# Kernel tuning notes

Hardware: AMD Instinct MI355X
Metric: run time of the kernel (lower is better)

The kernel has to match this reference:

```python
import jax, jax.numpy as jnp
import numpy as np

B, C, N, K = 2, 64, 16384, 16
C_OUT = 64


def setup_inputs() -> dict:
    key = jax.random.key(0)
    k1, k2, k3, k4 = jax.random.split(key, 4)
    x = jax.random.normal(k1, (B, C, N), dtype=jnp.float32)
    edge_index = jax.random.randint(k2, (2, B, N, K), 0, N, dtype=jnp.int64)
    # 1x1 Conv2d params: weight [C_out, 3C], bias [C_out]
    W = jax.random.normal(k3, (C_OUT, 3 * C), dtype=jnp.float32) * (1.0 / np.sqrt(3 * C))
    b = jax.random.normal(k4, (C_OUT,), dtype=jnp.float32) * 0.01
    return {"x": x, "edge_index": edge_index, "W": W, "b": b}


def _gather_nodes(x, idx):
    # x: [B, C, N], idx: [B, N, K] -> [B, C, N, K]
    return jax.vmap(lambda xb, ib: xb[:, ib])(x, idx)


def reference(x, edge_index, W, b):
    # x: [B, C, N]; edge_index: [2, B, N, K]
    x_i = _gather_nodes(x, edge_index[1])          # center features  [B,C,N,K]
    x_j = _gather_nodes(x, edge_index[0])          # neighbor features [B,C,N,K]
    edge_features = x_j - x_i                      # [B,C,N,K]
    global_feature = jnp.mean(x, axis=2, keepdims=True)  # [B,C,1] global mean over nodes
    global_rep = jnp.broadcast_to(global_feature[..., None], x_i.shape)  # [B,C,N,K]
    combined = jnp.concatenate([x_i, edge_features, global_rep], axis=1)  # [B,3C,N,K]
    # BasicConv: 1x1 conv + ReLU (norm=None)
    out = jnp.einsum("bcnk,oc->bonk", combined, W) + b[None, :, None, None]
    out = jax.nn.relu(out)
    return jnp.max(out, axis=-1, keepdims=True)    # [B,C_out,N,1]
```

## Files before the change

### kernel.cpp

```cpp
#include <hip/hip_runtime.h>
#include <hip/hip_bf16.h>


#define NNODES 16384
#define NCH 64

typedef _Float16 half4 __attribute__((ext_vector_type(4)));

__global__ __launch_bounds__(256) void mean_kernel(const float* __restrict__ x,
                                                   float* __restrict__ g) {
  int row = blockIdx.x;
  const float4* x4 = (const float4*)(x + (size_t)row * NNODES);
  int t = threadIdx.x;
  float s = 0.f;
#pragma unroll
  for (int i = 0; i < 16; ++i) {
    float4 q = x4[t + i * 256];
    s += (q.x + q.y) + (q.z + q.w);
  }
#pragma unroll
  for (int off = 32; off > 0; off >>= 1) s += __shfl_down(s, off, 64);
  __shared__ float wsum[4];
  int lane = t & 63, wv = t >> 6;
  if (lane == 0) wsum[wv] = s;
  __syncthreads();
  if (t == 0) g[row] = (wsum[0] + wsum[1] + wsum[2] + wsum[3]) * (1.0f / 16384.0f);
}

__global__ __launch_bounds__(128) void gmat_kernel(const float* __restrict__ W,
                                                   const float* __restrict__ bias,
                                                   const float* __restrict__ g,
                                                   float* __restrict__ G) {
  int t = threadIdx.x;
  int b = t >> 6, o = t & 63;
  float s = bias[o];
  const float* w3 = W + o * 192 + 128;
  const float* gb = g + b * 64;
#pragma unroll
  for (int c = 0; c < 64; ++c) s += w3[c] * gb[c];
  G[t] = s;
}

__global__ __launch_bounds__(256) void uv_kernel(const float* __restrict__ x,
                                                 const float* __restrict__ W,
                                                 _Float16* __restrict__ u,
                                                 _Float16* __restrict__ v) {
  __shared__ float A[64][64];
  __shared__ float Bm[64][64];
  int t = threadIdx.x;
  {
    int o = t & 63, c0 = (t >> 6) * 16;
    const float* wr = W + o * 192;
#pragma unroll
    for (int i = 0; i < 16; ++i) {
      int c = c0 + i;
      float w1 = wr[c], w2 = wr[64 + c];
      A[c][o] = w1 - w2;
      Bm[c][o] = w2;
    }
  }
  __syncthreads();
  int lane = t & 63;
  int wv = __builtin_amdgcn_readfirstlane(t >> 6);
  int blk = blockIdx.x;
  int b = blk >> 9;
  int m0 = (blk & 511) * 32 + wv * 8;
  const float* xb = x + (size_t)b * (NCH * NNODES) + m0;
  float aU[8], aV[8];
#pragma unroll
  for (int i = 0; i < 8; ++i) { aU[i] = 0.f; aV[i] = 0.f; }
#pragma unroll 8
  for (int c = 0; c < 64; ++c) {
    float a = A[c][lane];
    float bb = Bm[c][lane];
    const float4* xr = (const float4*)(xb + (size_t)c * NNODES);
    float4 q0 = xr[0];
    float4 q1 = xr[1];
    aU[0] += a * q0.x; aV[0] += bb * q0.x;
    aU[1] += a * q0.y; aV[1] += bb * q0.y;
    aU[2] += a * q0.z; aV[2] += bb * q0.z;
    aU[3] += a * q0.w; aV[3] += bb * q0.w;
    aU[4] += a * q1.x; aV[4] += bb * q1.x;
    aU[5] += a * q1.y; aV[5] += bb * q1.y;
    aU[6] += a * q1.z; aV[6] += bb * q1.z;
    aU[7] += a * q1.w; aV[7] += bb * q1.w;
  }
  _Float16* ub = u + ((size_t)b * NNODES + m0) * NCH + lane;
  _Float16* vb = v + ((size_t)b * NNODES + m0) * NCH + lane;
#pragma unroll
  for (int i = 0; i < 8; ++i) {
    ub[i * NCH] = (_Float16)aU[i];
    vb[i * NCH] = (_Float16)aV[i];
  }
}

__global__ __launch_bounds__(256) void gather_kernel(const int* __restrict__ ei,
                                                     const _Float16* __restrict__ u,
                                                     const _Float16* __restrict__ v,
                                                     const float* __restrict__ G,
                                                     float* __restrict__ out) {
  __shared__ float tile[64][17];
  int t = threadIdx.x;
  int lane = t & 63;
  int wv = t >> 6;
  int blk = blockIdx.x;
  int xcd = blk & 7;
  int b = xcd >> 2;
  int nb = (blk >> 3) * 4 + (xcd & 3);
  int n0 = nb * 16;
  int node_q = lane >> 4;
  int k_l = lane & 15;
  int n = n0 + wv * 4 + node_q;
  const int* e0b = ei + (size_t)b * NNODES * 16;
  const int* e1b = ei + (size_t)(2 + b) * NNODES * 16;
  int idx0 = e0b[n * 16 + k_l];
  int idx1 = e1b[n * 16 + k_l];
  int c4 = k_l * 4;
  const half4* ub = (const half4*)(u + (size_t)b * NNODES * NCH + c4);
  const half4* vb = (const half4*)(v + (size_t)b * NNODES * NCH + c4);
  half4 acc;
  acc.x = acc.y = acc.z = acc.w = (_Float16)(-60000.0f);
#pragma unroll
  for (int k = 0; k < 16; ++k) {
    int src = (lane & 48) + k;
    int m1 = __shfl(idx1, src, 64);
    int m0 = __shfl(idx0, src, 64);
    half4 a = ub[(size_t)m1 * 16];
    half4 bb = vb[(size_t)m0 * 16];
    half4 s = a + bb;
    acc = __builtin_elementwise_max(acc, s);
  }
  float4 Gl = *(const float4*)(G + b * 64 + c4);
  int nn = wv * 4 + node_q;
  tile[c4 + 0][nn] = fmaxf((float)acc.x + Gl.x, 0.0f);
  tile[c4 + 1][nn] = fmaxf((float)acc.y + Gl.y, 0.0f);
  tile[c4 + 2][nn] = fmaxf((float)acc.z + Gl.z, 0.0f);
  tile[c4 + 3][nn] = fmaxf((float)acc.w + Gl.w, 0.0f);
  __syncthreads();
  int col = t & 15;
  int orow = t >> 4;
#pragma unroll
  for (int j = 0; j < 4; ++j) {
    int o = orow + j * 16;
    out[((size_t)b * 64 + o) * NNODES + n0 + col] = tile[o][col];
  }
}

extern "C" void kernel_launch(void* const* d_in, const int* in_sizes, int n_in,
                              void* d_out, int out_size, void* d_ws, size_t ws_size,
                              hipStream_t stream) {
  const float* x = (const float*)d_in[0];
  const int* ei = (const int*)d_in[1];
  const float* W = (const float*)d_in[2];
  const float* bias = (const float*)d_in[3];
  float* out = (float*)d_out;

  char* ws = (char*)d_ws;
  _Float16* u = (_Float16*)ws;
  _Float16* v = (_Float16*)(ws + (size_t)4 * 1024 * 1024);
  float* g = (float*)(ws + (size_t)8 * 1024 * 1024);
  float* G = g + 256;

  mean_kernel<<<128, 256, 0, stream>>>(x, g);
  gmat_kernel<<<1, 128, 0, stream>>>(W, bias, g, G);
  uv_kernel<<<1024, 256, 0, stream>>>(x, W, u, v);
  gather_kernel<<<2048, 256, 0, stream>>>(ei, u, v, G, out);
}
```

Baseline: 96.68 us.

## Fuse global-term matvec into gather kernel and widen gathers to half8

Removes the separate single-block gmat kernel launch by recomputing the global-feature contribution W3·g + bias in every gather block through shared memory. The gather kernel now handles 32 nodes per block, with 8 lanes per node each loading 8 fp16 channels (16-byte loads) instead of 16 lanes loading 4 channels. This halves the grid and cuts shuffle and instruction overhead per gathered row. In exchange, each block redoes a small 64x64 matvec and adds two extra barriers.

```diff
diff --git a/kernel.cpp b/kernel.cpp
--- a/kernel.cpp
+++ b/kernel.cpp
@@ -5,7 +5,7 @@
 #define NNODES 16384
 #define NCH 64
 
-typedef _Float16 half4 __attribute__((ext_vector_type(4)));
+typedef _Float16 half8 __attribute__((ext_vector_type(8)));
 
 __global__ __launch_bounds__(256) void mean_kernel(const float* __restrict__ x,
                                                    float* __restrict__ g) {
@@ -25,20 +25,6 @@
   if (lane == 0) wsum[wv] = s;
   __syncthreads();
   if (t == 0) g[row] = (wsum[0] + wsum[1] + wsum[2] + wsum[3]) * (1.0f / 16384.0f);
-}
-
-__global__ __launch_bounds__(128) void gmat_kernel(const float* __restrict__ W,
-                                                   const float* __restrict__ bias,
-                                                   const float* __restrict__ g,
-                                                   float* __restrict__ G) {
-  int t = threadIdx.x;
-  int b = t >> 6, o = t & 63;
-  float s = bias[o];
-  const float* w3 = W + o * 192 + 128;
-  const float* gb = g + b * 64;
-#pragma unroll
-  for (int c = 0; c < 64; ++c) s += w3[c] * gb[c];
-  G[t] = s;
 }
 
 __global__ __launch_bounds__(256) void uv_kernel(const float* __restrict__ x,
@@ -97,9 +83,13 @@
 __global__ __launch_bounds__(256) void gather_kernel(const int* __restrict__ ei,
                                                      const _Float16* __restrict__ u,
                                                      const _Float16* __restrict__ v,
-                                                     const float* __restrict__ G,
+                                                     const float* __restrict__ W,
+                                                     const float* __restrict__ bias,
+                                                     const float* __restrict__ g,
                                                      float* __restrict__ out) {
-  __shared__ float tile[64][17];
+  __shared__ float tile[64][33];
+  __shared__ float pg[4][64];
+  __shared__ float G_s[64];
   int t = threadIdx.x;
   int lane = t & 63;
   int wv = t >> 6;
@@ -107,42 +97,58 @@
   int xcd = blk & 7;
   int b = xcd >> 2;
   int nb = (blk >> 3) * 4 + (xcd & 3);
-  int n0 = nb * 16;
-  int node_q = lane >> 4;
-  int k_l = lane & 15;
-  int n = n0 + wv * 4 + node_q;
+  int n0 = nb * 32;
+  int q = lane >> 3;
+  int r = lane & 7;
   const int* e0b = ei + (size_t)b * NNODES * 16;
   const int* e1b = ei + (size_t)(2 + b) * NNODES * 16;
-  int idx0 = e0b[n * 16 + k_l];
-  int idx1 = e1b[n * 16 + k_l];
-  int c4 = k_l * 4;
-  const half4* ub = (const half4*)(u + (size_t)b * NNODES * NCH + c4);
-  const half4* vb = (const half4*)(v + (size_t)b * NNODES * NCH + c4);
-  half4 acc;
-  acc.x = acc.y = acc.z = acc.w = (_Float16)(-60000.0f);
+  int f0 = (n0 + wv * 8) * 16 + q * 16 + r;
+  int i0a = e0b[f0];
+  int i0b = e0b[f0 + 8];
+  int i1a = e1b[f0];
+  int i1b = e1b[f0 + 8];
+  {
+    int o = t >> 2, cq = t & 3;
+    const float4* wr = (const float4*)(W + o * 192 + 128 + cq * 16);
+    const float4* gr = (const float4*)(g + b * 64 + cq * 16);
+    float s = 0.f;
+#pragma unroll
+    for (int j = 0; j < 4; ++j) {
+      float4 w = wr[j];
+      float4 gg = gr[j];
+      s += w.x * gg.x + w.y * gg.y + w.z * gg.z + w.w * gg.w;
+    }
+    pg[cq][o] = s;
+  }
+  __syncthreads();
+  if (t < 64) G_s[t] = bias[t] + ((pg[0][t] + pg[1][t]) + (pg[2][t] + pg[3][t]));
+  __syncthreads();
+  const half8* u8 = (const half8*)(u + (size_t)b * NNODES * NCH) + r;
+  const half8* v8 = (const half8*)(v + (size_t)b * NNODES * NCH) + r;
+  half8 acc;
+#pragma unroll
+  for (int j = 0; j < 8; ++j) acc[j] = (_Float16)(-60000.0f);
 #pragma unroll
   for (int k = 0; k < 16; ++k) {
-    int src = (lane & 48) + k;
-    int m1 = __shfl(idx1, src, 64);
-    int m0 = __shfl(idx0, src, 64);
-    half4 a = ub[(size_t)m1 * 16];
-    half4 bb = vb[(size_t)m0 * 16];
-    half4 s = a + bb;
+    int src = (lane & 56) + (k & 7);
+    int m1 = __shfl(k < 8 ? i1a : i1b, src, 64);
+    int m0 = __shfl(k < 8 ? i0a : i0b, src, 64);
+    half8 a = u8[(size_t)m1 * 8];
+    half8 bb = v8[(size_t)m0 * 8];
+    half8 s = a + bb;
     acc = __builtin_elementwise_max(acc, s);
   }
-  float4 Gl = *(const float4*)(G + b * 64 + c4);
-  int nn = wv * 4 + node_q;
-  tile[c4 + 0][nn] = fmaxf((float)acc.x + Gl.x, 0.0f);
-  tile[c4 + 1][nn] = fmaxf((float)acc.y + Gl.y, 0.0f);
-  tile[c4 + 2][nn] = fmaxf((float)acc.z + Gl.z, 0.0f);
-  tile[c4 + 3][nn] = fmaxf((float)acc.w + Gl.w, 0.0f);
+  int col = wv * 8 + q;
+#pragma unroll
+  for (int j = 0; j < 8; ++j) {
+    tile[r * 8 + j][col] = fmaxf((float)acc[j] + G_s[r * 8 + j], 0.0f);
+  }
   __syncthreads();
-  int col = t & 15;
-  int orow = t >> 4;
 #pragma unroll
-  for (int j = 0; j < 4; ++j) {
-    int o = orow + j * 16;
-    out[((size_t)b * 64 + o) * NNODES + n0 + col] = tile[o][col];
+  for (int j = 0; j < 8; ++j) {
+    int o = (t >> 5) + j * 8;
+    int c2 = t & 31;
+    out[((size_t)b * 64 + o) * NNODES + n0 + c2] = tile[o][c2];
   }
 }
 
@@ -159,10 +165,8 @@
   _Float16* u = (_Float16*)ws;
   _Float16* v = (_Float16*)(ws + (size_t)4 * 1024 * 1024);
   float* g = (float*)(ws + (size_t)8 * 1024 * 1024);
-  float* G = g + 256;
 
   mean_kernel<<<128, 256, 0, stream>>>(x, g);
-  gmat_kernel<<<1, 128, 0, stream>>>(W, bias, g, G);
   uv_kernel<<<1024, 256, 0, stream>>>(x, W, u, v);
-  gather_kernel<<<2048, 256, 0, stream>>>(ei, u, v, G, out);
+  gather_kernel<<<1024, 256, 0, stream>>>(ei, u, v, W, bias, g, out);
 }
```

After: 93.59 us. 3.2% less time.
